# Performance work log

Hardware: AMD Instinct MI355X
Metric: run time of the kernel (lower is better)

Reference implementation:

```python
import jax, jax.numpy as jnp
import numpy as np

N, D = 8192, 1024
Q = 4096
DK = 512
DV = 256


def setup_inputs() -> dict:
    key = jax.random.key(0)
    k1, k2, k3, k4, k5, k6 = jax.random.split(key, 6)
    return {
        "search_x": jax.random.normal(k1, (N, D), dtype=jnp.float32),
        "search_y": jax.random.normal(k2, (N, DV), dtype=jnp.float32),
        "query_x": jax.random.normal(k3, (Q, D), dtype=jnp.float32),
        "mask": jax.random.randint(k4, (Q, N), 0, 2, dtype=jnp.int64),
        "Wk": jax.random.normal(k5, (D, DK), dtype=jnp.float32) / np.sqrt(D),
        "Wq": jax.random.normal(k6, (D, DK), dtype=jnp.float32) / np.sqrt(D),
    }


def reference(search_x, search_y, query_x, mask, Wk, Wq):
    # key/query modules: bias-free linear projections (n_keys == 1 after _ensure_key_shape)
    keys = search_x @ Wk            # [N, DK]
    qk = query_x @ Wq               # [Q, DK]
    scale = 1.0 / jnp.sqrt(jnp.asarray(DK, dtype=keys.dtype))
    logits = (qk @ keys.T) * scale  # [Q, N]  (== broadcast mul+sum in original)
    # masked softmax over the search dimension (dim=1)
    m = mask > 0                    # [Q, N]
    neg = jnp.finfo(logits.dtype).min
    p = jax.nn.softmax(jnp.where(m, logits, neg), axis=1)
    p = jnp.where(m, p, 0.0)
    # values = noop_value_module(search_x, search_y) = search_y  [N, DV]
    res = p @ search_y              # [Q, DV]
    return res[:, None, :]          # [Q, n_keys=1, DV], matching original output shape
```

## Files before the change

kernel.cpp:

```cpp
#include <hip/hip_runtime.h>
#include <hip/hip_fp16.h>

typedef _Float16 half4v __attribute__((ext_vector_type(4)));
typedef _Float16 half8v __attribute__((ext_vector_type(8)));
typedef float floatx4 __attribute__((ext_vector_type(4)));

#define GLOBAL_AS __attribute__((address_space(1)))
#define LDS_AS __attribute__((address_space(3)))

__device__ __forceinline__ void async_copy16(const _Float16* g, _Float16* l) {
    __builtin_amdgcn_global_load_lds((const GLOBAL_AS unsigned int*)g,
                                     (LDS_AS unsigned int*)l, 16, 0, 0);
}

__global__ __launch_bounds__(256) void k_f32_to_f16(const float* __restrict__ in,
                                                    _Float16* __restrict__ out, int n) {
    int i = (blockIdx.x * 256 + threadIdx.x) * 4;
    if (i >= n) return;
    float4 v = *(const float4*)(in + i);
    half4v h;
    h[0] = (_Float16)v.x; h[1] = (_Float16)v.y; h[2] = (_Float16)v.z; h[3] = (_Float16)v.w;
    *(half4v*)(out + i) = h;
}

__global__ __launch_bounds__(256) void k_transpose_f16(const float* __restrict__ in,
                                                       _Float16* __restrict__ out,
                                                       int R, int C) {
    __shared__ float tile[32][33];
    int bc = blockIdx.x * 32;
    int br = blockIdx.y * 32;
    int tx = threadIdx.x & 31, ty = threadIdx.x >> 5;
#pragma unroll
    for (int i = 0; i < 32; i += 8)
        tile[ty + i][tx] = in[(size_t)(br + ty + i) * C + bc + tx];
    __syncthreads();
#pragma unroll
    for (int i = 0; i < 32; i += 8)
        out[(size_t)(bc + ty + i) * R + br + tx] = (_Float16)tile[tx][ty + i];
}

template <int OUT_MODE>
__global__ __launch_bounds__(256) void k_gemm_nt(const _Float16* __restrict__ A,
                                                 const _Float16* __restrict__ B,
                                                 void* __restrict__ C,
                                                 int M, int N, int K, int kChunk,
                                                 float scale) {
    __shared__ __align__(16) _Float16 As[128 * 64];
    __shared__ __align__(16) _Float16 Bs[128 * 64];
    const int tid  = threadIdx.x;
    const int lane = tid & 63;
    const int wave = tid >> 6;
    const int wm   = (wave >> 1) * 64;
    const int wn   = (wave & 1) * 64;
    const int quad = lane >> 4;
    const int lr   = lane & 15;
    const long m0 = (long)blockIdx.y * 128;
    const long n0 = (long)blockIdx.x * 128;
    const int kBegin = blockIdx.z * kChunk;
    const int kEnd   = kBegin + kChunk;

    floatx4 acc[4][4] = {};

    const int rl = lane >> 3;
    const int gc = (lane & 7) ^ rl;
    const long arow = m0 + wave * 32 + rl;
    const long brow = n0 + wave * 32 + rl;

    for (int kt = kBegin; kt < kEnd; kt += 64) {
        const _Float16* Ap = A + arow * (long)K + kt + gc * 8;
        const _Float16* Bp = B + brow * (long)K + kt + gc * 8;
        _Float16* Al = &As[(wave * 32) * 64];
        _Float16* Bl = &Bs[(wave * 32) * 64];
#pragma unroll
        for (int i = 0; i < 4; ++i) {
            async_copy16(Ap + (long)(i * 8) * K, Al + i * 8 * 64);
            async_copy16(Bp + (long)(i * 8) * K, Bl + i * 8 * 64);
        }
        __syncthreads();

#pragma unroll
        for (int kk = 0; kk < 64; kk += 32) {
            half8v af[4], bf[4];
            const int cg = (kk >> 3) + quad;
            const int sl = (cg ^ (lr & 7)) * 8;
#pragma unroll
            for (int i = 0; i < 4; ++i)
                af[i] = *(const half8v*)&As[(wm + i * 16 + lr) * 64 + sl];
#pragma unroll
            for (int j = 0; j < 4; ++j)
                bf[j] = *(const half8v*)&Bs[(wn + j * 16 + lr) * 64 + sl];
#pragma unroll
            for (int i = 0; i < 4; ++i)
#pragma unroll
                for (int j = 0; j < 4; ++j)
                    acc[i][j] = __builtin_amdgcn_mfma_f32_16x16x32_f16(af[i], bf[j], acc[i][j], 0, 0, 0);
        }
        __syncthreads();
    }

#pragma unroll
    for (int i = 0; i < 4; ++i) {
        long rbase = m0 + wm + i * 16 + quad * 4;
#pragma unroll
        for (int j = 0; j < 4; ++j) {
            long col = n0 + wn + j * 16 + lr;
#pragma unroll
            for (int r = 0; r < 4; ++r) {
                float val = acc[i][j][r] * scale;
                if (OUT_MODE == 0)
                    ((_Float16*)C)[(rbase + r) * (long)N + col] = (_Float16)val;
                else
                    ((float*)C)[(size_t)blockIdx.z * M * N + (rbase + r) * (long)N + col] = val;
            }
        }
    }
}

__global__ __launch_bounds__(256) void k_reduce8(const float* __restrict__ part,
                                                 float* __restrict__ out, int n) {
    int i = (blockIdx.x * 256 + threadIdx.x) * 4;
    if (i >= n) return;
    float4 s = *(const float4*)(part + i);
#pragma unroll
    for (int z = 1; z < 8; ++z) {
        float4 v = *(const float4*)(part + (size_t)z * n + i);
        s.x += v.x; s.y += v.y; s.z += v.z; s.w += v.w;
    }
    *(float4*)(out + i) = s;
}

__global__ __launch_bounds__(256) void k_softmax(_Float16* __restrict__ logits,
                                                 const int* __restrict__ mask) {
    const int q   = blockIdx.x;
    const int tid = threadIdx.x;
    _Float16* row   = logits + (size_t)q * 8192;
    const int* mrow = mask + (size_t)q * 8192;

    float v[32];
    unsigned mb = 0;
    float lmax = -3.0e38f;
#pragma unroll
    for (int i = 0; i < 8; ++i) {
        int base = i * 1024 + tid * 4;
        int4 mm  = *(const int4*)(mrow + base);
        half4v h = *(const half4v*)(row + base);
#pragma unroll
        for (int j = 0; j < 4; ++j) v[i * 4 + j] = (float)h[j];
        if (mm.x > 0) { mb |= 1u << (i * 4 + 0); lmax = fmaxf(lmax, v[i * 4 + 0]); }
        if (mm.y > 0) { mb |= 1u << (i * 4 + 1); lmax = fmaxf(lmax, v[i * 4 + 1]); }
        if (mm.z > 0) { mb |= 1u << (i * 4 + 2); lmax = fmaxf(lmax, v[i * 4 + 2]); }
        if (mm.w > 0) { mb |= 1u << (i * 4 + 3); lmax = fmaxf(lmax, v[i * 4 + 3]); }
    }
#pragma unroll
    for (int off = 32; off > 0; off >>= 1) lmax = fmaxf(lmax, __shfl_xor(lmax, off, 64));
    __shared__ float redmax[4], redsum[4];
    if ((tid & 63) == 0) redmax[tid >> 6] = lmax;
    __syncthreads();
    lmax = fmaxf(fmaxf(redmax[0], redmax[1]), fmaxf(redmax[2], redmax[3]));

    float lsum = 0.f;
#pragma unroll
    for (int i = 0; i < 32; ++i) {
        float e = ((mb >> i) & 1u) ? __expf(v[i] - lmax) : 0.f;
        v[i] = e;
        lsum += e;
    }
#pragma unroll
    for (int off = 32; off > 0; off >>= 1) lsum += __shfl_xor(lsum, off, 64);
    if ((tid & 63) == 0) redsum[tid >> 6] = lsum;
    __syncthreads();
    lsum = redsum[0] + redsum[1] + redsum[2] + redsum[3];
    float inv = lsum > 0.f ? 1.f / lsum : 0.f;

#pragma unroll
    for (int i = 0; i < 8; ++i) {
        int base = i * 1024 + tid * 4;
        half4v h;
#pragma unroll
        for (int j = 0; j < 4; ++j) h[j] = (_Float16)(v[i * 4 + j] * inv);
        *(half4v*)(row + base) = h;
    }
}

extern "C" void kernel_launch(void* const* d_in, const int* in_sizes, int n_in,
                              void* d_out, int out_size, void* d_ws, size_t ws_size,
                              hipStream_t stream) {
    const float* search_x = (const float*)d_in[0];
    const float* search_y = (const float*)d_in[1];
    const float* query_x  = (const float*)d_in[2];
    const int*   mask     = (const int*)d_in[3];
    const float* Wk       = (const float*)d_in[4];
    const float* Wq       = (const float*)d_in[5];
    (void)in_sizes; (void)n_in; (void)ws_size; (void)out_size;

    char* p = (char*)d_ws;
    _Float16* xh   = (_Float16*)p; p += (size_t)8192 * 1024 * 2;
    _Float16* qh   = (_Float16*)p; p += (size_t)4096 * 1024 * 2;
    _Float16* wkT  = (_Float16*)p; p += (size_t)512 * 1024 * 2;
    _Float16* wqT  = (_Float16*)p; p += (size_t)512 * 1024 * 2;
    _Float16* yT   = (_Float16*)p; p += (size_t)256 * 8192 * 2;
    _Float16* keys = (_Float16*)p; p += (size_t)8192 * 512 * 2;
    _Float16* qk   = (_Float16*)p; p += (size_t)4096 * 512 * 2;
    _Float16* lg   = (_Float16*)p; p += (size_t)4096 * 8192 * 2;
    float*    part = (float*)p;    p += (size_t)8 * 4096 * 256 * 4;

    k_f32_to_f16<<<8192, 256, 0, stream>>>(search_x, xh, 8192 * 1024);
    k_f32_to_f16<<<4096, 256, 0, stream>>>(query_x, qh, 4096 * 1024);
    k_transpose_f16<<<dim3(16, 32), 256, 0, stream>>>(Wk, wkT, 1024, 512);
    k_transpose_f16<<<dim3(16, 32), 256, 0, stream>>>(Wq, wqT, 1024, 512);
    k_transpose_f16<<<dim3(8, 256), 256, 0, stream>>>(search_y, yT, 8192, 256);

    k_gemm_nt<0><<<dim3(4, 64, 1), 256, 0, stream>>>(xh, wkT, keys, 8192, 512, 1024, 1024, 1.0f);
    k_gemm_nt<0><<<dim3(4, 32, 1), 256, 0, stream>>>(qh, wqT, qk, 4096, 512, 1024, 1024, 1.0f);
    k_gemm_nt<0><<<dim3(64, 32, 1), 256, 0, stream>>>(qk, keys, lg, 4096, 8192, 512, 512,
                                                      0.04419417382415922f);
    k_softmax<<<4096, 256, 0, stream>>>(lg, mask);
    k_gemm_nt<1><<<dim3(2, 32, 8), 256, 0, stream>>>(lg, yT, part, 4096, 256, 8192, 1024, 1.0f);
    k_reduce8<<<1024, 256, 0, stream>>>(part, (float*)d_out, 4096 * 256);
}
```

Before: 367.1 us.

## Fuse logits, masked softmax and PV GEMM into split-N flash attention kernel

Replaces the separate logits GEMM, masked softmax kernel and split-K PV GEMM with a flash-attention style kernel. Each block handles 64 queries over a 1024-key chunk, runs an online softmax in registers, and writes partial outputs plus running max and sum. A combine kernel then merges the 8 chunks. This removes the 64MB fp16 logits round-trip through global memory. In exchange it adds per-tile syncs and recomputes Q staging for every key tile, and the mask is read with scattered int loads from the fragment layout.

```diff
diff --git a/kernel.cpp b/kernel.cpp
--- a/kernel.cpp
+++ b/kernel.cpp
@@ -11,6 +11,18 @@
 __device__ __forceinline__ void async_copy16(const _Float16* g, _Float16* l) {
     __builtin_amdgcn_global_load_lds((const GLOBAL_AS unsigned int*)g,
                                      (LDS_AS unsigned int*)l, 16, 0, 0);
+}
+
+template <int R>
+__device__ __forceinline__ void stage_tile(const _Float16* g, long ldg,
+                                           _Float16* lds, int wave, int lane) {
+    const int rl = lane >> 3;
+    const int gc = (lane & 7) ^ rl;
+#pragma unroll
+    for (int i = 0; i < (R >> 5); ++i) {
+        const int br = wave * (R >> 2) + i * 8;
+        async_copy16(g + (long)(br + rl) * ldg + gc * 8, lds + br * 64);
+    }
 }
 
 __global__ __launch_bounds__(256) void k_f32_to_f16(const float* __restrict__ in,
@@ -39,56 +51,30 @@
         out[(size_t)(bc + ty + i) * R + br + tx] = (_Float16)tile[tx][ty + i];
 }
 
-template <int OUT_MODE>
 __global__ __launch_bounds__(256) void k_gemm_nt(const _Float16* __restrict__ A,
                                                  const _Float16* __restrict__ B,
-                                                 void* __restrict__ C,
-                                                 int M, int N, int K, int kChunk,
-                                                 float scale) {
+                                                 _Float16* __restrict__ C,
+                                                 int M, int N, int K) {
     __shared__ __align__(16) _Float16 As[128 * 64];
     __shared__ __align__(16) _Float16 Bs[128 * 64];
-    const int tid  = threadIdx.x;
-    const int lane = tid & 63;
-    const int wave = tid >> 6;
-    const int wm   = (wave >> 1) * 64;
-    const int wn   = (wave & 1) * 64;
-    const int quad = lane >> 4;
-    const int lr   = lane & 15;
-    const long m0 = (long)blockIdx.y * 128;
-    const long n0 = (long)blockIdx.x * 128;
-    const int kBegin = blockIdx.z * kChunk;
-    const int kEnd   = kBegin + kChunk;
+    const int tid = threadIdx.x, lane = tid & 63, wave = tid >> 6;
+    const int wm = (wave >> 1) * 64, wn = (wave & 1) * 64;
+    const int quad = lane >> 4, lr = lane & 15;
+    const long m0 = (long)blockIdx.y * 128, n0 = (long)blockIdx.x * 128;
 
     floatx4 acc[4][4] = {};
-
-    const int rl = lane >> 3;
-    const int gc = (lane & 7) ^ rl;
-    const long arow = m0 + wave * 32 + rl;
-    const long brow = n0 + wave * 32 + rl;
-
-    for (int kt = kBegin; kt < kEnd; kt += 64) {
-        const _Float16* Ap = A + arow * (long)K + kt + gc * 8;
-        const _Float16* Bp = B + brow * (long)K + kt + gc * 8;
-        _Float16* Al = &As[(wave * 32) * 64];
-        _Float16* Bl = &Bs[(wave * 32) * 64];
-#pragma unroll
-        for (int i = 0; i < 4; ++i) {
-            async_copy16(Ap + (long)(i * 8) * K, Al + i * 8 * 64);
-            async_copy16(Bp + (long)(i * 8) * K, Bl + i * 8 * 64);
-        }
+    for (int kt = 0; kt < K; kt += 64) {
+        stage_tile<128>(A + m0 * K + kt, K, As, wave, lane);
+        stage_tile<128>(B + n0 * K + kt, K, Bs, wave, lane);
         __syncthreads();
-
 #pragma unroll
         for (int kk = 0; kk < 64; kk += 32) {
+            const int sl = ((((kk >> 3) + quad) ^ (lr & 7)) * 8);
             half8v af[4], bf[4];
-            const int cg = (kk >> 3) + quad;
-            const int sl = (cg ^ (lr & 7)) * 8;
-#pragma unroll
-            for (int i = 0; i < 4; ++i)
-                af[i] = *(const half8v*)&As[(wm + i * 16 + lr) * 64 + sl];
-#pragma unroll
-            for (int j = 0; j < 4; ++j)
-                bf[j] = *(const half8v*)&Bs[(wn + j * 16 + lr) * 64 + sl];
+#pragma unroll
+            for (int i = 0; i < 4; ++i) af[i] = *(const half8v*)&As[(wm + i * 16 + lr) * 64 + sl];
+#pragma unroll
+            for (int j = 0; j < 4; ++j) bf[j] = *(const half8v*)&Bs[(wn + j * 16 + lr) * 64 + sl];
 #pragma unroll
             for (int i = 0; i < 4; ++i)
 #pragma unroll
@@ -97,7 +83,6 @@
         }
         __syncthreads();
     }
-
 #pragma unroll
     for (int i = 0; i < 4; ++i) {
         long rbase = m0 + wm + i * 16 + quad * 4;
@@ -105,81 +90,227 @@
         for (int j = 0; j < 4; ++j) {
             long col = n0 + wn + j * 16 + lr;
 #pragma unroll
-            for (int r = 0; r < 4; ++r) {
-                float val = acc[i][j][r] * scale;
-                if (OUT_MODE == 0)
-                    ((_Float16*)C)[(rbase + r) * (long)N + col] = (_Float16)val;
-                else
-                    ((float*)C)[(size_t)blockIdx.z * M * N + (rbase + r) * (long)N + col] = val;
-            }
-        }
-    }
-}
-
-__global__ __launch_bounds__(256) void k_reduce8(const float* __restrict__ part,
-                                                 float* __restrict__ out, int n) {
-    int i = (blockIdx.x * 256 + threadIdx.x) * 4;
-    if (i >= n) return;
-    float4 s = *(const float4*)(part + i);
-#pragma unroll
-    for (int z = 1; z < 8; ++z) {
-        float4 v = *(const float4*)(part + (size_t)z * n + i);
-        s.x += v.x; s.y += v.y; s.z += v.z; s.w += v.w;
-    }
-    *(float4*)(out + i) = s;
-}
-
-__global__ __launch_bounds__(256) void k_softmax(_Float16* __restrict__ logits,
-                                                 const int* __restrict__ mask) {
-    const int q   = blockIdx.x;
-    const int tid = threadIdx.x;
-    _Float16* row   = logits + (size_t)q * 8192;
-    const int* mrow = mask + (size_t)q * 8192;
-
-    float v[32];
-    unsigned mb = 0;
-    float lmax = -3.0e38f;
-#pragma unroll
-    for (int i = 0; i < 8; ++i) {
-        int base = i * 1024 + tid * 4;
-        int4 mm  = *(const int4*)(mrow + base);
-        half4v h = *(const half4v*)(row + base);
-#pragma unroll
-        for (int j = 0; j < 4; ++j) v[i * 4 + j] = (float)h[j];
-        if (mm.x > 0) { mb |= 1u << (i * 4 + 0); lmax = fmaxf(lmax, v[i * 4 + 0]); }
-        if (mm.y > 0) { mb |= 1u << (i * 4 + 1); lmax = fmaxf(lmax, v[i * 4 + 1]); }
-        if (mm.z > 0) { mb |= 1u << (i * 4 + 2); lmax = fmaxf(lmax, v[i * 4 + 2]); }
-        if (mm.w > 0) { mb |= 1u << (i * 4 + 3); lmax = fmaxf(lmax, v[i * 4 + 3]); }
-    }
-#pragma unroll
-    for (int off = 32; off > 0; off >>= 1) lmax = fmaxf(lmax, __shfl_xor(lmax, off, 64));
-    __shared__ float redmax[4], redsum[4];
-    if ((tid & 63) == 0) redmax[tid >> 6] = lmax;
-    __syncthreads();
-    lmax = fmaxf(fmaxf(redmax[0], redmax[1]), fmaxf(redmax[2], redmax[3]));
-
-    float lsum = 0.f;
-#pragma unroll
-    for (int i = 0; i < 32; ++i) {
-        float e = ((mb >> i) & 1u) ? __expf(v[i] - lmax) : 0.f;
-        v[i] = e;
-        lsum += e;
-    }
-#pragma unroll
-    for (int off = 32; off > 0; off >>= 1) lsum += __shfl_xor(lsum, off, 64);
-    if ((tid & 63) == 0) redsum[tid >> 6] = lsum;
-    __syncthreads();
-    lsum = redsum[0] + redsum[1] + redsum[2] + redsum[3];
-    float inv = lsum > 0.f ? 1.f / lsum : 0.f;
-
-#pragma unroll
-    for (int i = 0; i < 8; ++i) {
-        int base = i * 1024 + tid * 4;
-        half4v h;
-#pragma unroll
-        for (int j = 0; j < 4; ++j) h[j] = (_Float16)(v[i * 4 + j] * inv);
-        *(half4v*)(row + base) = h;
-    }
+            for (int r = 0; r < 4; ++r)
+                C[(rbase + r) * (long)N + col] = (_Float16)acc[i][j][r];
+        }
+    }
+}
+
+#define SCALE 0.04419417382415922f
+__global__ __launch_bounds__(256, 2) void k_flash(const _Float16* __restrict__ qk,
+                                                  const _Float16* __restrict__ keys,
+                                                  const _Float16* __restrict__ yT,
+                                                  const int* __restrict__ mask,
+                                                  float* __restrict__ part,
+                                                  float* __restrict__ ml) {
+    __shared__ __align__(16) char smem[50176];
+    _Float16* Qs = (_Float16*)smem;
+    _Float16* Ks = (_Float16*)(smem + 8192);
+    _Float16* Ps = (_Float16*)smem;
+    _Float16* Ys = (_Float16*)(smem + 17408);
+    __shared__ float s_max[2][64];
+    __shared__ float s_sum[2][64];
+
+    const int tid = threadIdx.x, lane = tid & 63, wave = tid >> 6;
+    const int wr = wave >> 1, wc = wave & 1;
+    const int quad = lane >> 4, lr = lane & 15;
+    const int nc = blockIdx.x;
+    const int q0 = blockIdx.y * 64;
+    const long n0 = (long)nc * 1024;
+
+    floatx4 acc_o[2][8] = {};
+    float m_reg[2][4], l_reg[2][4];
+#pragma unroll
+    for (int i = 0; i < 2; ++i)
+#pragma unroll
+        for (int r = 0; r < 4; ++r) { m_reg[i][r] = -3.0e38f; l_reg[i][r] = 0.f; }
+
+    const _Float16* Qg = qk + (long)q0 * 512;
+
+    for (int t = 0; t < 8; ++t) {
+        const _Float16* Kg = keys + (n0 + t * 128) * 512;
+        floatx4 acc_s[2][4] = {};
+        for (int kt = 0; kt < 512; kt += 64) {
+            stage_tile<64>(Qg + kt, 512, Qs, wave, lane);
+            stage_tile<128>(Kg + kt, 512, Ks, wave, lane);
+            __syncthreads();
+#pragma unroll
+            for (int kk = 0; kk < 64; kk += 32) {
+                const int sl = ((((kk >> 3) + quad) ^ (lr & 7)) * 8);
+                half8v af[2], bf[4];
+#pragma unroll
+                for (int i = 0; i < 2; ++i)
+                    af[i] = *(const half8v*)&Qs[(wr * 32 + i * 16 + lr) * 64 + sl];
+#pragma unroll
+                for (int j = 0; j < 4; ++j)
+                    bf[j] = *(const half8v*)&Ks[(wc * 64 + j * 16 + lr) * 64 + sl];
+#pragma unroll
+                for (int i = 0; i < 2; ++i)
+#pragma unroll
+                    for (int j = 0; j < 4; ++j)
+                        acc_s[i][j] = __builtin_amdgcn_mfma_f32_16x16x32_f16(af[i], bf[j], acc_s[i][j], 0, 0, 0);
+            }
+            __syncthreads();
+        }
+        float val[2][4][4], rmax[2][4];
+#pragma unroll
+        for (int i = 0; i < 2; ++i)
+#pragma unroll
+            for (int r = 0; r < 4; ++r) rmax[i][r] = -3.0e38f;
+#pragma unroll
+        for (int i = 0; i < 2; ++i)
+#pragma unroll
+            for (int j = 0; j < 4; ++j) {
+                const int col = wc * 64 + j * 16 + lr;
+#pragma unroll
+                for (int r = 0; r < 4; ++r) {
+                    const int row = wr * 32 + i * 16 + quad * 4 + r;
+                    const int mk = mask[(size_t)(q0 + row) * 8192 + n0 + t * 128 + col];
+                    float v = (mk > 0) ? acc_s[i][j][r] * SCALE : -3.0e38f;
+                    val[i][j][r] = v;
+                    rmax[i][r] = fmaxf(rmax[i][r], v);
+                }
+            }
+#pragma unroll
+        for (int i = 0; i < 2; ++i)
+#pragma unroll
+            for (int r = 0; r < 4; ++r) {
+#pragma unroll
+                for (int m = 1; m < 16; m <<= 1)
+                    rmax[i][r] = fmaxf(rmax[i][r], __shfl_xor(rmax[i][r], m, 64));
+            }
+        if (lr == 0) {
+#pragma unroll
+            for (int i = 0; i < 2; ++i)
+#pragma unroll
+                for (int r = 0; r < 4; ++r)
+                    s_max[wc][wr * 32 + i * 16 + quad * 4 + r] = rmax[i][r];
+        }
+        __syncthreads();
+        float mnew[2][4], alpha[2][4], rsum[2][4];
+#pragma unroll
+        for (int i = 0; i < 2; ++i)
+#pragma unroll
+            for (int r = 0; r < 4; ++r) {
+                const int row = wr * 32 + i * 16 + quad * 4 + r;
+                float mt = fmaxf(s_max[0][row], s_max[1][row]);
+                mnew[i][r] = fmaxf(m_reg[i][r], mt);
+                alpha[i][r] = __expf(m_reg[i][r] - mnew[i][r]);
+                m_reg[i][r] = mnew[i][r];
+                rsum[i][r] = 0.f;
+            }
+#pragma unroll
+        for (int i = 0; i < 2; ++i)
+#pragma unroll
+            for (int j = 0; j < 4; ++j) {
+                const int col = wc * 64 + j * 16 + lr;
+#pragma unroll
+                for (int r = 0; r < 4; ++r) {
+                    const int row = wr * 32 + i * 16 + quad * 4 + r;
+                    float p = (val[i][j][r] > -1.0e37f) ? __expf(val[i][j][r] - mnew[i][r]) : 0.f;
+                    rsum[i][r] += p;
+                    Ps[row * 136 + col] = (_Float16)p;
+                }
+            }
+#pragma unroll
+        for (int i = 0; i < 2; ++i)
+#pragma unroll
+            for (int j = 0; j < 8; ++j)
+#pragma unroll
+                for (int r = 0; r < 4; ++r) acc_o[i][j][r] *= alpha[i][r];
+#pragma unroll
+        for (int i = 0; i < 2; ++i)
+#pragma unroll
+            for (int r = 0; r < 4; ++r) {
+#pragma unroll
+                for (int m = 1; m < 16; m <<= 1)
+                    rsum[i][r] += __shfl_xor(rsum[i][r], m, 64);
+            }
+        if (lr == 0) {
+#pragma unroll
+            for (int i = 0; i < 2; ++i)
+#pragma unroll
+                for (int r = 0; r < 4; ++r)
+                    s_sum[wc][wr * 32 + i * 16 + quad * 4 + r] = rsum[i][r];
+        }
+        __syncthreads();
+#pragma unroll
+        for (int i = 0; i < 2; ++i)
+#pragma unroll
+            for (int r = 0; r < 4; ++r) {
+                const int row = wr * 32 + i * 16 + quad * 4 + r;
+                l_reg[i][r] = l_reg[i][r] * alpha[i][r] + s_sum[0][row] + s_sum[1][row];
+            }
+        const _Float16* Yg = yT + n0 + t * 128;
+#pragma unroll
+        for (int kk2 = 0; kk2 < 128; kk2 += 64) {
+            stage_tile<256>(Yg + kk2, 8192, Ys, wave, lane);
+            __syncthreads();
+#pragma unroll
+            for (int kkk = 0; kkk < 64; kkk += 32) {
+                const int sl = ((((kkk >> 3) + quad) ^ (lr & 7)) * 8);
+                half8v pa[2];
+#pragma unroll
+                for (int i = 0; i < 2; ++i)
+                    pa[i] = *(const half8v*)&Ps[(wr * 32 + i * 16 + lr) * 136 + kk2 + kkk + quad * 8];
+#pragma unroll
+                for (int j = 0; j < 8; ++j) {
+                    half8v yb = *(const half8v*)&Ys[(wc * 128 + j * 16 + lr) * 64 + sl];
+                    acc_o[0][j] = __builtin_amdgcn_mfma_f32_16x16x32_f16(pa[0], yb, acc_o[0][j], 0, 0, 0);
+                    acc_o[1][j] = __builtin_amdgcn_mfma_f32_16x16x32_f16(pa[1], yb, acc_o[1][j], 0, 0, 0);
+                }
+            }
+            __syncthreads();
+        }
+    }
+    float* op = part + ((size_t)nc * 4096 + q0) * 256;
+#pragma unroll
+    for (int i = 0; i < 2; ++i)
+#pragma unroll
+        for (int j = 0; j < 8; ++j) {
+            const int col = wc * 128 + j * 16 + lr;
+#pragma unroll
+            for (int r = 0; r < 4; ++r) {
+                const int row = wr * 32 + i * 16 + quad * 4 + r;
+                op[(long)row * 256 + col] = acc_o[i][j][r];
+            }
+        }
+    if (wc == 0 && lr == 0) {
+#pragma unroll
+        for (int i = 0; i < 2; ++i)
+#pragma unroll
+            for (int r = 0; r < 4; ++r) {
+                const int row = wr * 32 + i * 16 + quad * 4 + r;
+                ml[(size_t)nc * 4096 + q0 + row] = m_reg[i][r];
+                ml[32768 + (size_t)nc * 4096 + q0 + row] = l_reg[i][r];
+            }
+    }
+}
+
+__global__ __launch_bounds__(256) void k_combine(const float* __restrict__ part,
+                                                 const float* __restrict__ ml,
+                                                 float* __restrict__ out) {
+    const int q = blockIdx.x * 4 + (threadIdx.x >> 6);
+    const int c = (threadIdx.x & 63) * 4;
+    float mz[8], lz[8], M = -3.0e38f;
+#pragma unroll
+    for (int z = 0; z < 8; ++z) {
+        mz[z] = ml[(size_t)z * 4096 + q];
+        lz[z] = ml[32768 + (size_t)z * 4096 + q];
+        M = fmaxf(M, mz[z]);
+    }
+    float L = 0.f;
+    float4 o = make_float4(0.f, 0.f, 0.f, 0.f);
+#pragma unroll
+    for (int z = 0; z < 8; ++z) {
+        float w = __expf(mz[z] - M);
+        L += w * lz[z];
+        float4 v = *(const float4*)(part + ((size_t)z * 4096 + q) * 256 + c);
+        o.x += w * v.x; o.y += w * v.y; o.z += w * v.z; o.w += w * v.w;
+    }
+    float inv = (L > 0.f) ? 1.f / L : 0.f;
+    o.x *= inv; o.y *= inv; o.z *= inv; o.w *= inv;
+    *(float4*)(out + (size_t)q * 256 + c) = o;
 }
 
 extern "C" void kernel_launch(void* const* d_in, const int* in_sizes, int n_in,
@@ -201,8 +332,8 @@
     _Float16* yT   = (_Float16*)p; p += (size_t)256 * 8192 * 2;
     _Float16* keys = (_Float16*)p; p += (size_t)8192 * 512 * 2;
     _Float16* qk   = (_Float16*)p; p += (size_t)4096 * 512 * 2;
-    _Float16* lg   = (_Float16*)p; p += (size_t)4096 * 8192 * 2;
     float*    part = (float*)p;    p += (size_t)8 * 4096 * 256 * 4;
+    float*    ml   = (float*)p;    p += (size_t)2 * 8 * 4096 * 4;
 
     k_f32_to_f16<<<8192, 256, 0, stream>>>(search_x, xh, 8192 * 1024);
     k_f32_to_f16<<<4096, 256, 0, stream>>>(query_x, qh, 4096 * 1024);
@@ -210,11 +341,9 @@
     k_transpose_f16<<<dim3(16, 32), 256, 0, stream>>>(Wq, wqT, 1024, 512);
     k_transpose_f16<<<dim3(8, 256), 256, 0, stream>>>(search_y, yT, 8192, 256);
 
-    k_gemm_nt<0><<<dim3(4, 64, 1), 256, 0, stream>>>(xh, wkT, keys, 8192, 512, 1024, 1024, 1.0f);
-    k_gemm_nt<0><<<dim3(4, 32, 1), 256, 0, stream>>>(qh, wqT, qk, 4096, 512, 1024, 1024, 1.0f);
-    k_gemm_nt<0><<<dim3(64, 32, 1), 256, 0, stream>>>(qk, keys, lg, 4096, 8192, 512, 512,
-                                                      0.04419417382415922f);
-    k_softmax<<<4096, 256, 0, stream>>>(lg, mask);
-    k_gemm_nt<1><<<dim3(2, 32, 8), 256, 0, stream>>>(lg, yT, part, 4096, 256, 8192, 1024, 1.0f);
-    k_reduce8<<<1024, 256, 0, stream>>>(part, (float*)d_out, 4096 * 256);
-}
+    k_gemm_nt<<<dim3(4, 64), 256, 0, stream>>>(xh, wkT, keys, 8192, 512, 1024);
+    k_gemm_nt<<<dim3(4, 32), 256, 0, stream>>>(qh, wqT, qk, 4096, 512, 1024);
+
+    k_flash<<<dim3(8, 64), 256, 0, stream>>>(qk, keys, yT, mask, part, ml);
+    k_combine<<<1024, 256, 0, stream>>>(part, ml, (float*)d_out);
+}
```

Result: slower. 464.6 us (+26.6%).

## Fuse prep kernels, bit-pack mask, merge double-buffered projection GEMMs

Applied to the files above, without the earlier changes.

Merges the fp32-to-fp16 conversions and transposes into a single prep kernel. The same kernel packs the integer mask into a bitmask via wave ballots, so softmax reads 1 bit per element instead of 4 bytes. The two projection GEMMs become one launch with double-buffered LDS staging, which overlaps global loads with MFMA work. This cuts launch count and mask traffic in softmax, at the cost of a larger LDS footprint and a long serial loop per prep block. The mask is still read once in full, now inside prep.

```diff
diff --git a/kernel.cpp b/kernel.cpp
--- a/kernel.cpp
+++ b/kernel.cpp
@@ -13,23 +13,22 @@
                                      (LDS_AS unsigned int*)l, 16, 0, 0);
 }
 
-__global__ __launch_bounds__(256) void k_f32_to_f16(const float* __restrict__ in,
-                                                    _Float16* __restrict__ out, int n) {
-    int i = (blockIdx.x * 256 + threadIdx.x) * 4;
-    if (i >= n) return;
-    float4 v = *(const float4*)(in + i);
-    half4v h;
-    h[0] = (_Float16)v.x; h[1] = (_Float16)v.y; h[2] = (_Float16)v.z; h[3] = (_Float16)v.w;
-    *(half4v*)(out + i) = h;
-}
-
-__global__ __launch_bounds__(256) void k_transpose_f16(const float* __restrict__ in,
-                                                       _Float16* __restrict__ out,
-                                                       int R, int C) {
-    __shared__ float tile[32][33];
-    int bc = blockIdx.x * 32;
-    int br = blockIdx.y * 32;
-    int tx = threadIdx.x & 31, ty = threadIdx.x >> 5;
+template <int R>
+__device__ __forceinline__ void stage_tile(const _Float16* g, long ldg,
+                                           _Float16* lds, int wave, int lane) {
+    const int rl = lane >> 3;
+    const int gc = (lane & 7) ^ rl;
+#pragma unroll
+    for (int i = 0; i < (R >> 5); ++i) {
+        const int br = wave * (R >> 2) + i * 8;
+        async_copy16(g + (long)(br + rl) * ldg + gc * 8, lds + br * 64);
+    }
+}
+
+__device__ __forceinline__ void tr_tile(const float* __restrict__ in,
+                                        _Float16* __restrict__ out, int R, int C,
+                                        int br, int bc, int tid, float (*tile)[33]) {
+    int tx = tid & 31, ty = tid >> 5;
 #pragma unroll
     for (int i = 0; i < 32; i += 8)
         tile[ty + i][tx] = in[(size_t)(br + ty + i) * C + bc + tx];
@@ -37,6 +36,116 @@
 #pragma unroll
     for (int i = 0; i < 32; i += 8)
         out[(size_t)(bc + ty + i) * R + br + tx] = (_Float16)tile[tx][ty + i];
+    __syncthreads();
+}
+
+__global__ __launch_bounds__(256) void k_prep(
+    const float* __restrict__ search_x, const float* __restrict__ search_y,
+    const float* __restrict__ query_x, const int* __restrict__ mask,
+    const float* __restrict__ Wk, const float* __restrict__ Wq,
+    _Float16* __restrict__ xh, _Float16* __restrict__ qh,
+    _Float16* __restrict__ wkT, _Float16* __restrict__ wqT,
+    _Float16* __restrict__ yT, unsigned int* __restrict__ bm) {
+    __shared__ float tile[32][33];
+    const int bx = blockIdx.x, tid = threadIdx.x;
+    if (bx < 2048) {
+        const int gw = bx * 4 + (tid >> 6);
+        const int lane = tid & 63;
+        for (int it = 0; it < 64; ++it) {
+            const int idx = (gw * 64 + it) * 64 + lane;
+            const int v = mask[idx];
+            unsigned long long b = __ballot(v > 0);
+            if (lane == 0) bm[idx >> 5] = (unsigned int)b;
+            if (lane == 32) bm[idx >> 5] = (unsigned int)(b >> 32);
+        }
+    } else if (bx < 2560) {
+        const int base0 = (bx - 2048) * 256 + tid;
+        for (int it = 0; it < 16; ++it) {
+            const int i = (it * 512 * 256 + base0) * 4;
+            float4 v = *(const float4*)(search_x + i);
+            half4v h; h[0]=(_Float16)v.x; h[1]=(_Float16)v.y; h[2]=(_Float16)v.z; h[3]=(_Float16)v.w;
+            *(half4v*)(xh + i) = h;
+        }
+    } else if (bx < 2816) {
+        const int base0 = (bx - 2560) * 256 + tid;
+        for (int it = 0; it < 16; ++it) {
+            const int i = (it * 256 * 256 + base0) * 4;
+            float4 v = *(const float4*)(query_x + i);
+            half4v h; h[0]=(_Float16)v.x; h[1]=(_Float16)v.y; h[2]=(_Float16)v.z; h[3]=(_Float16)v.w;
+            *(half4v*)(qh + i) = h;
+        }
+    } else if (bx < 2944) {
+        for (int it = 0; it < 16; ++it) {
+            const int t = (bx - 2816) * 16 + it;
+            tr_tile(search_y, yT, 8192, 256, (t >> 3) * 32, (t & 7) * 32, tid, tile);
+        }
+    } else if (bx < 2976) {
+        for (int it = 0; it < 16; ++it) {
+            const int t = (bx - 2944) * 16 + it;
+            tr_tile(Wk, wkT, 1024, 512, (t >> 4) * 32, (t & 15) * 32, tid, tile);
+        }
+    } else {
+        for (int it = 0; it < 16; ++it) {
+            const int t = (bx - 2976) * 16 + it;
+            tr_tile(Wq, wqT, 1024, 512, (t >> 4) * 32, (t & 15) * 32, tid, tile);
+        }
+    }
+}
+
+__global__ __launch_bounds__(256, 2) void k_proj(const _Float16* __restrict__ xh,
+                                                 const _Float16* __restrict__ qh,
+                                                 const _Float16* __restrict__ wkT,
+                                                 const _Float16* __restrict__ wqT,
+                                                 _Float16* __restrict__ keys,
+                                                 _Float16* __restrict__ qk) {
+    __shared__ __align__(16) _Float16 As[2][128 * 64];
+    __shared__ __align__(16) _Float16 Bs[2][128 * 64];
+    const int tid = threadIdx.x, lane = tid & 63, wave = tid >> 6;
+    const int wm = (wave >> 1) * 64, wn = (wave & 1) * 64;
+    const int quad = lane >> 4, lr = lane & 15;
+    const bool isK = blockIdx.y < 64;
+    const _Float16* A = isK ? xh : qh;
+    const _Float16* B = isK ? wkT : wqT;
+    _Float16* C = isK ? keys : qk;
+    const long m0 = (long)(isK ? blockIdx.y : blockIdx.y - 64) * 128;
+    const long n0 = (long)blockIdx.x * 128;
+
+    floatx4 acc[4][4] = {};
+    stage_tile<128>(A + m0 * 1024, 1024, As[0], wave, lane);
+    stage_tile<128>(B + n0 * 1024, 1024, Bs[0], wave, lane);
+    for (int ktI = 0; ktI < 16; ++ktI) {
+        __syncthreads();
+        const int cb = ktI & 1;
+        if (ktI < 15) {
+            stage_tile<128>(A + m0 * 1024 + (ktI + 1) * 64, 1024, As[cb ^ 1], wave, lane);
+            stage_tile<128>(B + n0 * 1024 + (ktI + 1) * 64, 1024, Bs[cb ^ 1], wave, lane);
+        }
+#pragma unroll
+        for (int kk = 0; kk < 64; kk += 32) {
+            const int sl = ((((kk >> 3) + quad) ^ (lr & 7)) * 8);
+            half8v af[4], bf[4];
+#pragma unroll
+            for (int i = 0; i < 4; ++i) af[i] = *(const half8v*)&As[cb][(wm + i * 16 + lr) * 64 + sl];
+#pragma unroll
+            for (int j = 0; j < 4; ++j) bf[j] = *(const half8v*)&Bs[cb][(wn + j * 16 + lr) * 64 + sl];
+#pragma unroll
+            for (int i = 0; i < 4; ++i)
+#pragma unroll
+                for (int j = 0; j < 4; ++j)
+                    acc[i][j] = __builtin_amdgcn_mfma_f32_16x16x32_f16(af[i], bf[j], acc[i][j], 0, 0, 0);
+        }
+    }
+#pragma unroll
+    for (int i = 0; i < 4; ++i) {
+        long rbase = m0 + wm + i * 16 + quad * 4;
+#pragma unroll
+        for (int j = 0; j < 4; ++j) {
+            long col = n0 + wn + j * 16 + lr;
+#pragma unroll
+            for (int r = 0; r < 4; ++r)
+                C[(rbase + r) * 512 + col] = (_Float16)acc[i][j][r];
+        }
+    }
 }
 
 template <int OUT_MODE>
@@ -47,48 +156,26 @@
                                                  float scale) {
     __shared__ __align__(16) _Float16 As[128 * 64];
     __shared__ __align__(16) _Float16 Bs[128 * 64];
-    const int tid  = threadIdx.x;
-    const int lane = tid & 63;
-    const int wave = tid >> 6;
-    const int wm   = (wave >> 1) * 64;
-    const int wn   = (wave & 1) * 64;
-    const int quad = lane >> 4;
-    const int lr   = lane & 15;
-    const long m0 = (long)blockIdx.y * 128;
-    const long n0 = (long)blockIdx.x * 128;
+    const int tid = threadIdx.x, lane = tid & 63, wave = tid >> 6;
+    const int wm = (wave >> 1) * 64, wn = (wave & 1) * 64;
+    const int quad = lane >> 4, lr = lane & 15;
+    const long m0 = (long)blockIdx.y * 128, n0 = (long)blockIdx.x * 128;
     const int kBegin = blockIdx.z * kChunk;
     const int kEnd   = kBegin + kChunk;
 
     floatx4 acc[4][4] = {};
-
-    const int rl = lane >> 3;
-    const int gc = (lane & 7) ^ rl;
-    const long arow = m0 + wave * 32 + rl;
-    const long brow = n0 + wave * 32 + rl;
-
     for (int kt = kBegin; kt < kEnd; kt += 64) {
-        const _Float16* Ap = A + arow * (long)K + kt + gc * 8;
-        const _Float16* Bp = B + brow * (long)K + kt + gc * 8;
-        _Float16* Al = &As[(wave * 32) * 64];
-        _Float16* Bl = &Bs[(wave * 32) * 64];
-#pragma unroll
-        for (int i = 0; i < 4; ++i) {
-            async_copy16(Ap + (long)(i * 8) * K, Al + i * 8 * 64);
-            async_copy16(Bp + (long)(i * 8) * K, Bl + i * 8 * 64);
-        }
+        stage_tile<128>(A + m0 * K + kt, K, As, wave, lane);
+        stage_tile<128>(B + n0 * K + kt, K, Bs, wave, lane);
         __syncthreads();
-
 #pragma unroll
         for (int kk = 0; kk < 64; kk += 32) {
+            const int sl = ((((kk >> 3) + quad) ^ (lr & 7)) * 8);
             half8v af[4], bf[4];
-            const int cg = (kk >> 3) + quad;
-            const int sl = (cg ^ (lr & 7)) * 8;
-#pragma unroll
-            for (int i = 0; i < 4; ++i)
-                af[i] = *(const half8v*)&As[(wm + i * 16 + lr) * 64 + sl];
-#pragma unroll
-            for (int j = 0; j < 4; ++j)
-                bf[j] = *(const half8v*)&Bs[(wn + j * 16 + lr) * 64 + sl];
+#pragma unroll
+            for (int i = 0; i < 4; ++i) af[i] = *(const half8v*)&As[(wm + i * 16 + lr) * 64 + sl];
+#pragma unroll
+            for (int j = 0; j < 4; ++j) bf[j] = *(const half8v*)&Bs[(wn + j * 16 + lr) * 64 + sl];
 #pragma unroll
             for (int i = 0; i < 4; ++i)
 #pragma unroll
@@ -97,7 +184,6 @@
         }
         __syncthreads();
     }
-
 #pragma unroll
     for (int i = 0; i < 4; ++i) {
         long rbase = m0 + wm + i * 16 + quad * 4;
@@ -116,6 +202,61 @@
     }
 }
 
+__global__ __launch_bounds__(256) void k_softmax(_Float16* __restrict__ logits,
+                                                 const unsigned int* __restrict__ bm) {
+    const int q   = blockIdx.x;
+    const int tid = threadIdx.x;
+    _Float16* row = logits + (size_t)q * 8192;
+    const unsigned int* bmr = bm + (size_t)q * 256;
+
+    float v[32];
+    unsigned mb = 0;
+    float lmax = -3.0e38f;
+#pragma unroll
+    for (int i = 0; i < 8; ++i) {
+        int base = i * 1024 + tid * 4;
+        half4v h = *(const half4v*)(row + base);
+        unsigned bits = (bmr[base >> 5] >> ((tid & 7) * 4)) & 0xFu;
+#pragma unroll
+        for (int j = 0; j < 4; ++j) {
+            v[i * 4 + j] = (float)h[j];
+            if ((bits >> j) & 1u) {
+                mb |= 1u << (i * 4 + j);
+                lmax = fmaxf(lmax, v[i * 4 + j]);
+            }
+        }
+    }
+#pragma unroll
+    for (int off = 32; off > 0; off >>= 1) lmax = fmaxf(lmax, __shfl_xor(lmax, off, 64));
+    __shared__ float redmax[4], redsum[4];
+    if ((tid & 63) == 0) redmax[tid >> 6] = lmax;
+    __syncthreads();
+    lmax = fmaxf(fmaxf(redmax[0], redmax[1]), fmaxf(redmax[2], redmax[3]));
+
+    float lsum = 0.f;
+#pragma unroll
+    for (int i = 0; i < 32; ++i) {
+        float e = ((mb >> i) & 1u) ? __expf(v[i] - lmax) : 0.f;
+        v[i] = e;
+        lsum += e;
+    }
+#pragma unroll
+    for (int off = 32; off > 0; off >>= 1) lsum += __shfl_xor(lsum, off, 64);
+    if ((tid & 63) == 0) redsum[tid >> 6] = lsum;
+    __syncthreads();
+    lsum = redsum[0] + redsum[1] + redsum[2] + redsum[3];
+    float inv = lsum > 0.f ? 1.f / lsum : 0.f;
+
+#pragma unroll
+    for (int i = 0; i < 8; ++i) {
+        int base = i * 1024 + tid * 4;
+        half4v h;
+#pragma unroll
+        for (int j = 0; j < 4; ++j) h[j] = (_Float16)(v[i * 4 + j] * inv);
+        *(half4v*)(row + base) = h;
+    }
+}
+
 __global__ __launch_bounds__(256) void k_reduce8(const float* __restrict__ part,
                                                  float* __restrict__ out, int n) {
     int i = (blockIdx.x * 256 + threadIdx.x) * 4;
@@ -127,59 +268,6 @@
         s.x += v.x; s.y += v.y; s.z += v.z; s.w += v.w;
     }
     *(float4*)(out + i) = s;
-}
-
-__global__ __launch_bounds__(256) void k_softmax(_Float16* __restrict__ logits,
-                                                 const int* __restrict__ mask) {
-    const int q   = blockIdx.x;
-    const int tid = threadIdx.x;
-    _Float16* row   = logits + (size_t)q * 8192;
-    const int* mrow = mask + (size_t)q * 8192;
-
-    float v[32];
-    unsigned mb = 0;
-    float lmax = -3.0e38f;
-#pragma unroll
-    for (int i = 0; i < 8; ++i) {
-        int base = i * 1024 + tid * 4;
-        int4 mm  = *(const int4*)(mrow + base);
-        half4v h = *(const half4v*)(row + base);
-#pragma unroll
-        for (int j = 0; j < 4; ++j) v[i * 4 + j] = (float)h[j];
-        if (mm.x > 0) { mb |= 1u << (i * 4 + 0); lmax = fmaxf(lmax, v[i * 4 + 0]); }
-        if (mm.y > 0) { mb |= 1u << (i * 4 + 1); lmax = fmaxf(lmax, v[i * 4 + 1]); }
-        if (mm.z > 0) { mb |= 1u << (i * 4 + 2); lmax = fmaxf(lmax, v[i * 4 + 2]); }
-        if (mm.w > 0) { mb |= 1u << (i * 4 + 3); lmax = fmaxf(lmax, v[i * 4 + 3]); }
-    }
-#pragma unroll
-    for (int off = 32; off > 0; off >>= 1) lmax = fmaxf(lmax, __shfl_xor(lmax, off, 64));
-    __shared__ float redmax[4], redsum[4];
-    if ((tid & 63) == 0) redmax[tid >> 6] = lmax;
-    __syncthreads();
-    lmax = fmaxf(fmaxf(redmax[0], redmax[1]), fmaxf(redmax[2], redmax[3]));
-
-    float lsum = 0.f;
-#pragma unroll
-    for (int i = 0; i < 32; ++i) {
-        float e = ((mb >> i) & 1u) ? __expf(v[i] - lmax) : 0.f;
-        v[i] = e;
-        lsum += e;
-    }
-#pragma unroll
-    for (int off = 32; off > 0; off >>= 1) lsum += __shfl_xor(lsum, off, 64);
-    if ((tid & 63) == 0) redsum[tid >> 6] = lsum;
-    __syncthreads();
-    lsum = redsum[0] + redsum[1] + redsum[2] + redsum[3];
-    float inv = lsum > 0.f ? 1.f / lsum : 0.f;
-
-#pragma unroll
-    for (int i = 0; i < 8; ++i) {
-        int base = i * 1024 + tid * 4;
-        half4v h;
-#pragma unroll
-        for (int j = 0; j < 4; ++j) h[j] = (_Float16)(v[i * 4 + j] * inv);
-        *(half4v*)(row + base) = h;
-    }
 }
 
 extern "C" void kernel_launch(void* const* d_in, const int* in_sizes, int n_in,
@@ -201,20 +289,16 @@
     _Float16* yT   = (_Float16*)p; p += (size_t)256 * 8192 * 2;
     _Float16* keys = (_Float16*)p; p += (size_t)8192 * 512 * 2;
     _Float16* qk   = (_Float16*)p; p += (size_t)4096 * 512 * 2;
+    unsigned int* bmw = (unsigned int*)p; p += (size_t)4096 * 256 * 4;
     _Float16* lg   = (_Float16*)p; p += (size_t)4096 * 8192 * 2;
     float*    part = (float*)p;    p += (size_t)8 * 4096 * 256 * 4;
 
-    k_f32_to_f16<<<8192, 256, 0, stream>>>(search_x, xh, 8192 * 1024);
-    k_f32_to_f16<<<4096, 256, 0, stream>>>(query_x, qh, 4096 * 1024);
-    k_transpose_f16<<<dim3(16, 32), 256, 0, stream>>>(Wk, wkT, 1024, 512);
-    k_transpose_f16<<<dim3(16, 32), 256, 0, stream>>>(Wq, wqT, 1024, 512);
-    k_transpose_f16<<<dim3(8, 256), 256, 0, stream>>>(search_y, yT, 8192, 256);
-
-    k_gemm_nt<0><<<dim3(4, 64, 1), 256, 0, stream>>>(xh, wkT, keys, 8192, 512, 1024, 1024, 1.0f);
-    k_gemm_nt<0><<<dim3(4, 32, 1), 256, 0, stream>>>(qh, wqT, qk, 4096, 512, 1024, 1024, 1.0f);
+    k_prep<<<3008, 256, 0, stream>>>(search_x, search_y, query_x, mask, Wk, Wq,
+                                     xh, qh, wkT, wqT, yT, bmw);
+    k_proj<<<dim3(4, 96), 256, 0, stream>>>(xh, qh, wkT, wqT, keys, qk);
     k_gemm_nt<0><<<dim3(64, 32, 1), 256, 0, stream>>>(qk, keys, lg, 4096, 8192, 512, 512,
                                                       0.04419417382415922f);
-    k_softmax<<<4096, 256, 0, stream>>>(lg, mask);
+    k_softmax<<<4096, 256, 0, stream>>>(lg, bmw);
     k_gemm_nt<1><<<dim3(2, 32, 8), 256, 0, stream>>>(lg, yT, part, 4096, 256, 8192, 1024, 1.0f);
     k_reduce8<<<1024, 256, 0, stream>>>(part, (float*)d_out, 4096 * 256);
 }
```

Result: slower. 414.5 us (+12.9%).
